# Kernel optimization log

Measured on AMD Instinct MI355X. Metric: run time of the kernel, lower is better.

The kernel has to match this reference:

```python
import jax, jax.numpy as jnp
import numpy as np

UNITS = 128
INPUT_DIM = 784
OUTPUT_DIM = 10
NUM_LAYERS = 8
BATCH = 2048
DT = 0.1
EPS = 0.01
TOL = 1e-4
STEPS = 15


def setup_inputs() -> dict:
    key = jax.random.key(0)
    k = jax.random.split(key, 7)
    s_in = 1.0 / np.sqrt(INPUT_DIM)
    s_u = 1.0 / np.sqrt(UNITS)
    return {
        "x": jax.random.normal(k[0], (BATCH, INPUT_DIM), jnp.float32),
        "w_in": jax.random.uniform(k[1], (UNITS, INPUT_DIM), jnp.float32, -s_in, s_in),
        "b_in": jax.random.uniform(k[2], (UNITS,), jnp.float32, -s_in, s_in),
        "w_blocks": jax.random.uniform(k[3], (NUM_LAYERS, UNITS, UNITS), jnp.float32, -s_u, s_u),
        "b_blocks": jax.random.uniform(k[4], (NUM_LAYERS, UNITS), jnp.float32, -s_u, s_u),
        "w_out": jax.random.uniform(k[5], (OUTPUT_DIM, UNITS), jnp.float32, -s_u, s_u),
        "b_out": jax.random.uniform(k[6], (OUTPUT_DIM,), jnp.float32, -s_u, s_u),
    }


def _build_A(w_blocks):
    # A_l = [[I, dt*W_l], [-dt*W_l^T, (1+dt/eps)*I]], shape [L, 2u, 2u]
    I = jnp.broadcast_to(jnp.eye(UNITS, dtype=w_blocks.dtype), (NUM_LAYERS, UNITS, UNITS))
    top = jnp.concatenate([I, DT * w_blocks], axis=2)
    bot = jnp.concatenate([-DT * jnp.transpose(w_blocks, (0, 2, 1)), (1.0 + DT / EPS) * I], axis=2)
    return jnp.concatenate([top, bot], axis=1)


def _sweep(z_in, A, b_blocks):
    # Fixed-point sweeping (no-grad region in the original). z_ls: [L, B, 2u]
    B = z_in.shape[0]

    def layer_step(z, xs):
        A_l, b_l, z_l = xs
        rhs = jnp.concatenate(
            [jnp.broadcast_to(DT * b_l, (B, UNITS)), (DT / EPS) * jnp.tanh(z_l[:, :UNITS])],
            axis=1,
        ) + z
        # A_l is shared across the batch: one LU, many rhs
        y = jnp.linalg.solve(A_l, rhs.T).T
        err = jnp.mean(jnp.linalg.norm(z_l - y, axis=1))
        return y, (y, err)

    def body(state):
        z_ls, _, step = state
        _, (new_zls, errs) = jax.lax.scan(layer_step, z_in, (A, b_blocks, z_ls))
        return (new_zls, jnp.mean(errs), step + 1)

    def cond(state):
        _, err, step = state
        return jnp.logical_and(step < STEPS, err > TOL)

    z0 = jnp.broadcast_to(z_in[None], (NUM_LAYERS,) + z_in.shape)
    z_ls, _, _ = jax.lax.while_loop(cond, body, (z0, jnp.float32(10.0), jnp.int32(0)))
    return z_ls


def _block(z_in, W, b, z_l):
    # implicit_forward of one TransNetLayerSweeping (z_l is the converged sweep state)
    u_l, v_l = z_l[:, :UNITS], z_l[:, UNITS:]
    u_out = -DT * (v_l @ W.T) + z_in[:, :UNITS] + DT * b
    v_out = DT * (u_l @ W) + z_in[:, UNITS:] - (DT / EPS) * (v_l - jnp.tanh(u_l))
    return jnp.concatenate([u_out, v_out], axis=1)


def reference(x, w_in, b_in, w_blocks, b_blocks, w_out, b_out):
    x1 = x @ w_in.T + b_in                                  # [B, u]
    z_in = jnp.concatenate([x1, jnp.tanh(x1)], axis=1)      # [B, 2u]
    z_ls = _sweep(z_in, _build_A(w_blocks), b_blocks)       # [L, B, 2u]
    # Original loop does z = block.implicit_forward(z_in) for every block,
    # so only the LAST block's output survives.
    z_out = _block(z_in, w_blocks[-1], b_blocks[-1], z_ls[-1])
    logits = z_out[:, :UNITS] @ w_out.T + b_out             # [B, out]
    return jax.nn.softmax(logits, axis=1)
```

## Files before the change

kernel.cpp:

```cpp
#include <hip/hip_runtime.h>

#define U 128
#define BATCH 2048
#define NL 8
#define NS 8
#define DTc 0.1f
#define TENf 10.0f
#define INVC (1.0f/11.0f)
#define AFACT (0.01f/11.0f)
#define AST 264

typedef unsigned short u16;
typedef __attribute__((ext_vector_type(8))) short bf16x8;
typedef __attribute__((ext_vector_type(4))) float f32x4;
#define MFMA16(a,b,c) __builtin_amdgcn_mfma_f32_16x16x32_bf16(a,b,c,0,0,0)

__device__ __forceinline__ float bf2f(u16 h){ return __uint_as_float(((unsigned int)h)<<16); }
__device__ __forceinline__ u16 f2bf(float f){
  unsigned int u = __float_as_uint(f);
  u += 0x7FFFu + ((u >> 16) & 1u);
  return (u16)(u >> 16);
}
__device__ __forceinline__ float fast_tanh(float x){
  float e = __expf(2.0f*x);
  return 1.0f - __fdividef(2.0f, e + 1.0f);
}
__device__ __forceinline__ int detect_md(const u16* x, int* s_bad, int t, int nthr){
  if(t==0) *s_bad = 0;
  __syncthreads();
  int f=0;
  for(int i=t;i<4096;i+=nthr){ float v = bf2f(x[i]); if(!(fabsf(v)<16.0f)) f=1; }
  if(f) atomicOr(s_bad,1);
  __syncthreads();
  return *s_bad ? 0 : 1;
}
__device__ __forceinline__ bf16x8 ld8f(const float* p){
  float4 f0 = *(const float4*)p, f1 = *(const float4*)(p+4);
  bf16x8 v;
  v[0]=(short)f2bf(f0.x); v[1]=(short)f2bf(f0.y); v[2]=(short)f2bf(f0.z); v[3]=(short)f2bf(f0.w);
  v[4]=(short)f2bf(f1.x); v[5]=(short)f2bf(f1.y); v[6]=(short)f2bf(f1.z); v[7]=(short)f2bf(f1.w);
  return v;
}
__device__ __forceinline__ void lgkm_barrier(){
  __builtin_amdgcn_sched_barrier(0);
  asm volatile("s_waitcnt lgkmcnt(0)\n\ts_barrier" ::: "memory");
  __builtin_amdgcn_sched_barrier(0);
}

__global__ __launch_bounds__(256) void convK(
    const void* __restrict__ xraw, const void* __restrict__ wb,
    u16* __restrict__ Wg, u16* __restrict__ Wtg){
  __shared__ int s_bad;
  const int t = threadIdx.x;
  const int md = detect_md((const u16*)xraw, &s_bad, t, 256);
  const int g = blockIdx.x*256 + t, GS = gridDim.x*256;
  for(int i=g;i<131072;i+=GS){
    u16 h = md ? ((const u16*)wb)[i] : f2bf(((const float*)wb)[i]);
    Wg[i] = h;
    int L = i>>14, j = i & 16383;
    Wtg[(L<<14) + (j&127)*U + (j>>7)] = h;
  }
}

template<typename EPI>
__device__ __forceinline__ void tile16(const u16* __restrict__ A, int lda,
                                       const u16* __restrict__ B, int ldb, EPI epi){
  const int lane = threadIdx.x & 63, w = threadIdx.x >> 6;
  const int ln = lane & 15, lq = lane >> 4;
  const int n0 = 32*w + ln, n1 = n0 + 16;
  bf16x8 af[4], b0[4], b1[4];
  #pragma unroll
  for(int kt=0;kt<4;kt++){
    af[kt] = *(const bf16x8*)&A[ln*lda + kt*32 + lq*8];
    b0[kt] = *(const bf16x8*)&B[n0*ldb + kt*32 + lq*8];
    b1[kt] = *(const bf16x8*)&B[n1*ldb + kt*32 + lq*8];
  }
  f32x4 a0 = {0,0,0,0}, a1 = {0,0,0,0};
  #pragma unroll
  for(int kt=0;kt<4;kt++){ a0 = MFMA16(af[kt], b0[kt], a0); a1 = MFMA16(af[kt], b1[kt], a1); }
  epi(a0, a1, n0, n1);
}

__global__ __launch_bounds__(256) void gemmP(const u16* __restrict__ Wtg, u16* __restrict__ Pg){
  const int L = blockIdx.x >> 3, mt = blockIdx.x & 7;
  const int lq = (threadIdx.x & 63) >> 4;
  const u16* WtL = Wtg + (L<<14);
  tile16(WtL + mt*16*U, U, WtL, U, [&](f32x4 a0, f32x4 a1, int n0, int n1){
    #pragma unroll
    for(int r=0;r<4;r++){
      int row = mt*16 + lq*4 + r;
      Pg[(L<<14) + row*U + n0] = f2bf(AFACT*a0[r]);
      Pg[(L<<14) + row*U + n1] = f2bf(AFACT*a1[r]);
    }
  });
}
__global__ __launch_bounds__(256) void gemmS(const u16* __restrict__ Pg, u16* __restrict__ Fb){
  const int L = blockIdx.x >> 3, mt = blockIdx.x & 7;
  const int lq = (threadIdx.x & 63) >> 4;
  const u16* PL = Pg + (L<<14);
  u16* FbL = Fb + (size_t)L*65536;
  tile16(PL + mt*16*U, U, PL, U, [&](f32x4 a0, f32x4 a1, int n0, int n1){
    #pragma unroll
    for(int r=0;r<4;r++){
      int row = mt*16 + lq*4 + r;
      FbL[row*256 + n0] = f2bf(INVC*(((row==n0)?1.0f:0.0f) - bf2f(PL[row*U+n0]) + a0[r]));
      FbL[row*256 + n1] = f2bf(INVC*(((row==n1)?1.0f:0.0f) - bf2f(PL[row*U+n1]) + a1[r]));
    }
  });
}
__global__ __launch_bounds__(256) void gemmQ(const u16* __restrict__ Fb, const u16* __restrict__ Wg,
                                             u16* __restrict__ FbW){
  const int L = blockIdx.x >> 3, mt = blockIdx.x & 7;
  const int lq = (threadIdx.x & 63) >> 4;
  const u16* FbL = Fb + (size_t)L*65536;
  u16* FbO = FbW + (size_t)L*65536;
  tile16(FbL + mt*16*256, 256, Wg + (L<<14), U, [&](f32x4 a0, f32x4 a1, int n0, int n1){
    #pragma unroll
    for(int r=0;r<4;r++){
      int row = mt*16 + lq*4 + r;
      u16 q0 = f2bf(DTc*a0[r]), q1 = f2bf(DTc*a1[r]);
      FbO[row*256 + 128 + n0] = q0;
      FbO[row*256 + 128 + n1] = q1;
      FbO[(128+n0)*256 + row] = q0;
      FbO[(128+n1)*256 + row] = q1;
    }
  });
}
__global__ __launch_bounds__(256) void gemmR(const u16* __restrict__ Wg, u16* __restrict__ Fb){
  const int L = blockIdx.x >> 3, mt = blockIdx.x & 7;
  const int lq = (threadIdx.x & 63) >> 4;
  u16* FbL = Fb + (size_t)L*65536;
  tile16(Wg + (L<<14) + mt*16*U, U, FbL + 128*256, 256, [&](f32x4 a0, f32x4 a1, int n0, int n1){
    #pragma unroll
    for(int r=0;r<4;r++){
      int row = mt*16 + lq*4 + r;
      FbL[(128+row)*256 + 128 + n0] = f2bf(DTc*a0[r]);
      FbL[(128+row)*256 + 128 + n1] = f2bf(DTc*a1[r]);
    }
  });
}
__global__ __launch_bounds__(256) void swizK(const u16* __restrict__ Fb, u16* __restrict__ Fsw){
  const int L = blockIdx.x >> 3, part = blockIdx.x & 7;
  const u16* FbL = Fb + (size_t)L*65536;
  for(int i = part*1024 + threadIdx.x; i < (part+1)*1024; i += 256){
    int lanei = i & 63, kt = (i>>6)&7, c = (i>>9)&3, w = (i>>11)&3;
    int lni = lanei & 15, lqi = lanei >> 4;
    int row_n = 64*w + 16*c + lni;
    int col_k = kt*32 + lqi*8;
    *(bf16x8*)&Fsw[((size_t)L*8192 + i)*8] = *(const bf16x8*)&FbL[row_n*256 + col_k];
  }
}

__global__ __launch_bounds__(1024,1) void mainK(
    const void* __restrict__ xraw, const void* __restrict__ w_in,
    const void* __restrict__ b_in, const void* __restrict__ bb,
    const bf16x8* __restrict__ Fsw, const void* __restrict__ w_out,
    const void* __restrict__ b_out, void* __restrict__ outraw){
  __shared__ u16 At[2][16*AST];
  __shared__ u16 zh16[NL][16][132];
  __shared__ float zinu[16*U];
  __shared__ float bbL[NL*U];
  __shared__ float lg[16*12];
  __shared__ int s_bad;
  float* uout = (float*)&At[0][0];

  const int t = threadIdx.x;
  const int lane = t & 63, wid = t >> 6, ln = lane & 15, lq = lane >> 4;
  const int r0 = blockIdx.x * 16;

  const int md = detect_md((const u16*)xraw, &s_bad, t, 1024);
  for(int i=t;i<NL*U;i+=1024)
    bbL[i] = DTc * (md ? bf2f(((const u16*)bb)[i]) : ((const float*)bb)[i]);
  __syncthreads();

  if(wid < 8){
    const int n0 = 16*wid + ln;
    const u16*   wrb = (const u16*)w_in   + (size_t)n0*784;
    const float* wrf = (const float*)w_in + (size_t)n0*784;
    const u16*   xrb = (const u16*)xraw   + (size_t)(r0+ln)*784;
    const float* xrf = (const float*)xraw + (size_t)(r0+ln)*784;
    f32x4 acc = {0,0,0,0};
    const bf16x8 z8 = {0,0,0,0,0,0,0,0};
    if(md){
      #pragma unroll
      for(int kt=0; kt<24; ++kt){
        int k0 = kt*32 + lq*8;
        acc = MFMA16(*(const bf16x8*)(xrb + k0), *(const bf16x8*)(wrb + k0), acc);
      }
      { int k0 = 768 + lq*8;
        bf16x8 av = z8, bv = z8;
        if(lq < 2){ av = *(const bf16x8*)(xrb + k0); bv = *(const bf16x8*)(wrb + k0); }
        acc = MFMA16(av, bv, acc);
      }
    } else {
      #pragma unroll 4
      for(int kt=0; kt<24; ++kt){
        int k0 = kt*32 + lq*8;
        acc = MFMA16(ld8f(xrf + k0), ld8f(wrf + k0), acc);
      }
      { int k0 = 768 + lq*8;
        bf16x8 av = z8, bv = z8;
        if(lq < 2){ av = ld8f(xrf + k0); bv = ld8f(wrf + k0); }
        acc = MFMA16(av, bv, acc);
      }
    }
    float bi = md ? bf2f(((const u16*)b_in)[n0]) : ((const float*)b_in)[n0];
    #pragma unroll
    for(int r=0;r<4;r++) zinu[(lq*4+r)*U + n0] = acc[r] + bi;
  }
  __syncthreads();

  for(int i=t; i<NL*16*128; i+=1024){
    int l = i>>11, row = (i>>7)&15, c = i & 127;
    zh16[l][row][c] = f2bf(zinu[row*U + c]);
  }
  float ru[4];
  if(wid < 8){
    const int n = 16*wid + ln;
    #pragma unroll
    for(int r=0;r<4;r++){
      int row = lq*4 + r;
      At[0][row*AST + n] = f2bf((TENf + 1.0f) * fast_tanh(zinu[row*U + n]));
    }
  } else {
    const int uc = 16*(wid-8) + ln;
    #pragma unroll
    for(int r=0;r<4;r++){
      int row = lq*4 + r;
      float v = zinu[row*U + uc] + bbL[uc];
      ru[r] = v;
      At[0][row*AST + 128 + uc] = f2bf(v);
    }
  }
  const bf16x8* fbase = Fsw + (wid>>2)*2048 + (wid&3)*512 + lane;
  bf16x8 BfA[8], BfB[8];
  #pragma unroll
  for(int kt=0;kt<8;kt++) BfA[kt] = fbase[kt*64];
  __syncthreads();

#define STEPBODY(STEPV, BC, BN, CURC) { \
    const int l = (STEPV) & 7; \
    const int lnext = (l+1) & 7; \
    const bool last = ((STEPV) == NS*NL-1); \
    { const bf16x8* fp = fbase + lnext*8192; \
      _Pragma("unroll") \
      for(int kt=0;kt<8;kt++) BN[kt] = fp[kt*64]; } \
    bf16x8 at8[8]; \
    _Pragma("unroll") \
    for(int kt=0;kt<8;kt++) at8[kt] = *(const bf16x8*)&At[CURC][ln*AST + kt*32 + lq*8]; \
    float th[4]; \
    if(wid < 8 && !last){ \
      _Pragma("unroll") \
      for(int r=0;r<4;r++) th[r] = TENf * fast_tanh(bf2f(zh16[lnext][lq*4 + r][16*wid + ln])); \
    } \
    f32x4 acc = {0,0,0,0}; \
    _Pragma("unroll") \
    for(int kt=0;kt<8;kt++) acc = MFMA16(at8[kt], BC[kt], acc); \
    if(wid < 8){ \
      if(!last){ \
        const bool wrap = (l == 7); \
        const int n = 16*wid + ln; \
        _Pragma("unroll") \
        for(int r=0;r<4;r++){ \
          int row = lq*4 + r; \
          float base = wrap ? fast_tanh(zinu[row*U + n]) : acc[r]; \
          At[1-(CURC)][row*AST + n] = f2bf(th[r] + base); \
        } \
      } \
    } else { \
      const int uc0 = 16*(wid-8) + ln; \
      _Pragma("unroll") \
      for(int r=0;r<4;r++){ \
        int row = lq*4 + r; \
        float yu = ru[r] - acc[r]; \
        zh16[l][row][uc0] = f2bf(yu); \
        if(last){ \
          uout[row*U + uc0] = zinu[row*U + uc0] + bbL[7*U + uc0] - acc[r]; \
        } else if(l == 7){ \
          float rn = zinu[row*U + uc0] + bbL[uc0]; \
          ru[r] = rn; \
          At[1-(CURC)][row*AST + 128 + uc0] = f2bf(rn); \
        } else { \
          float rn = yu + bbL[(l+1)*U + uc0]; \
          ru[r] = rn; \
          At[1-(CURC)][row*AST + 128 + uc0] = f2bf(rn); \
        } \
      } \
    } \
    lgkm_barrier(); \
  }

  for(int sp=0; sp<NS*NL; sp+=2){
    STEPBODY(sp,   BfA, BfB, 0)
    STEPBODY(sp+1, BfB, BfA, 1)
  }
#undef STEPBODY

  if(t < 160){
    int mm = t/10, o = t - mm*10;
    float a = md ? bf2f(((const u16*)b_out)[o]) : ((const float*)b_out)[o];
    if(md){
      const u16* wo = (const u16*)w_out + o*U;
      for(int k=0;k<U;k++) a += uout[mm*U + k]*bf2f(wo[k]);
    } else {
      const float* wo = (const float*)w_out + o*U;
      for(int k=0;k<U;k++) a += uout[mm*U + k]*wo[k];
    }
    lg[mm*12 + o] = a;
  }
  __syncthreads();
  if(t < 16){
    float mx = -1e30f;
    for(int o=0;o<10;o++) mx = fmaxf(mx, lg[t*12 + o]);
    float e[10]; float sum = 0.0f;
    for(int o=0;o<10;o++){ e[o] = __expf(lg[t*12 + o] - mx); sum += e[o]; }
    float inv = 1.0f / sum;
    for(int o=0;o<10;o++){
      float pv = e[o]*inv;
      if(md) ((u16*)outraw)[(size_t)(r0 + t)*10 + o] = f2bf(pv);
      else   ((float*)outraw)[(size_t)(r0 + t)*10 + o] = pv;
    }
  }
}

extern "C" void kernel_launch(void* const* d_in, const int* in_sizes, int n_in,
                              void* d_out, int out_size, void* d_ws, size_t ws_size,
                              hipStream_t stream) {
  char* p = (char*)d_ws;
  u16* Fb      = (u16*)p;  p += (size_t)8*256*256*2;
  u16* Fsw     = (u16*)p;  p += (size_t)8*256*256*2;
  u16* Wg      = (u16*)p;  p += (size_t)8*128*128*2;
  u16* Wtg     = (u16*)p;  p += (size_t)8*128*128*2;
  u16* Pg      = (u16*)p;  p += (size_t)8*128*128*2;

  convK<<<128, 256, 0, stream>>>(d_in[0], d_in[3], Wg, Wtg);
  gemmP<<<64, 256, 0, stream>>>(Wtg, Pg);
  gemmS<<<64, 256, 0, stream>>>(Pg, Fb);
  gemmQ<<<64, 256, 0, stream>>>(Fb, Wg, Fb);
  gemmR<<<64, 256, 0, stream>>>(Wg, Fb);
  swizK<<<64, 256, 0, stream>>>(Fb, Fsw);
  mainK<<<BATCH/16, 1024, 0, stream>>>(d_in[0], d_in[1], d_in[2], d_in[4],
                                       (const bf16x8*)Fsw, d_in[5], d_in[6], d_out);
}
```

Before: 203.2 us.

## Fuse weight-prep kernels into one persistent kernel with grid barriers

Merges the six small preprocessing launches (convert, three GEMM stages, assemble, swizzle) into one 64-block kernel. The stages are separated by atomic-counter global barriers that are reset with a memset before each launch. The aim is to cut per-launch overhead and the idle gaps between tiny kernels. It also raises mainK's launch_bounds occupancy hint from 1 to 4, which may limit registers. The spin barrier assumes all 64 blocks are co-resident and adds an extra memset.

```diff
diff --git a/kernel.cpp b/kernel.cpp
--- a/kernel.cpp
+++ b/kernel.cpp
@@ -9,6 +9,7 @@
 #define INVC (1.0f/11.0f)
 #define AFACT (0.01f/11.0f)
 #define AST 264
+#define PREP_BLKS 64
 
 typedef unsigned short u16;
 typedef __attribute__((ext_vector_type(8))) short bf16x8;
@@ -47,19 +48,16 @@
   __builtin_amdgcn_sched_barrier(0);
 }
 
-__global__ __launch_bounds__(256) void convK(
-    const void* __restrict__ xraw, const void* __restrict__ wb,
-    u16* __restrict__ Wg, u16* __restrict__ Wtg){
-  __shared__ int s_bad;
-  const int t = threadIdx.x;
-  const int md = detect_md((const u16*)xraw, &s_bad, t, 256);
-  const int g = blockIdx.x*256 + t, GS = gridDim.x*256;
-  for(int i=g;i<131072;i+=GS){
-    u16 h = md ? ((const u16*)wb)[i] : f2bf(((const float*)wb)[i]);
-    Wg[i] = h;
-    int L = i>>14, j = i & 16383;
-    Wtg[(L<<14) + (j&127)*U + (j>>7)] = h;
-  }
+__device__ __forceinline__ void gbar(unsigned* cnt, int idx){
+  __syncthreads();
+  if(threadIdx.x==0){
+    __threadfence();
+    unsigned old = __hip_atomic_fetch_add(&cnt[idx], 1u, __ATOMIC_ACQ_REL, __HIP_MEMORY_SCOPE_AGENT);
+    unsigned tgt = (old/PREP_BLKS + 1u)*PREP_BLKS;
+    while(__hip_atomic_load(&cnt[idx], __ATOMIC_ACQUIRE, __HIP_MEMORY_SCOPE_AGENT) < tgt)
+      __builtin_amdgcn_s_sleep(4);
+  }
+  __syncthreads();
 }
 
 template<typename EPI>
@@ -81,24 +79,41 @@
   epi(a0, a1, n0, n1);
 }
 
-__global__ __launch_bounds__(256) void gemmP(const u16* __restrict__ Wtg, u16* __restrict__ Pg){
-  const int L = blockIdx.x >> 3, mt = blockIdx.x & 7;
-  const int lq = (threadIdx.x & 63) >> 4;
+__global__ __launch_bounds__(256) void prepK(
+    const void* __restrict__ xraw, const void* __restrict__ wb,
+    u16* __restrict__ Wg, u16* __restrict__ Wtg, u16* __restrict__ Pg,
+    u16* __restrict__ Fb, u16* __restrict__ Fsw, unsigned* __restrict__ cnt){
+  __shared__ int s_bad;
+  const int t = threadIdx.x, bid = blockIdx.x;
+  const int md = detect_md((const u16*)xraw, &s_bad, t, 256);
+
+  {
+    const int g = bid*256 + t, GS = PREP_BLKS*256;
+    for(int i=g;i<131072;i+=GS){
+      u16 h = md ? ((const u16*)wb)[i] : f2bf(((const float*)wb)[i]);
+      Wg[i] = h;
+      int L = i>>14, j = i & 16383;
+      Wtg[(L<<14) + (j&127)*U + (j>>7)] = h;
+    }
+  }
+  gbar(cnt, 0);
+
+  const int L = bid >> 3, mt = bid & 7;
+  const int lq = (t & 63) >> 4;
   const u16* WtL = Wtg + (L<<14);
+  u16* PL  = Pg + (L<<14);
+  u16* FbL = Fb + (size_t)L*65536;
+
   tile16(WtL + mt*16*U, U, WtL, U, [&](f32x4 a0, f32x4 a1, int n0, int n1){
     #pragma unroll
     for(int r=0;r<4;r++){
       int row = mt*16 + lq*4 + r;
-      Pg[(L<<14) + row*U + n0] = f2bf(AFACT*a0[r]);
-      Pg[(L<<14) + row*U + n1] = f2bf(AFACT*a1[r]);
+      PL[row*U + n0] = f2bf(AFACT*a0[r]);
+      PL[row*U + n1] = f2bf(AFACT*a1[r]);
     }
   });
-}
-__global__ __launch_bounds__(256) void gemmS(const u16* __restrict__ Pg, u16* __restrict__ Fb){
-  const int L = blockIdx.x >> 3, mt = blockIdx.x & 7;
-  const int lq = (threadIdx.x & 63) >> 4;
-  const u16* PL = Pg + (L<<14);
-  u16* FbL = Fb + (size_t)L*65536;
+  gbar(cnt, 1);
+
   tile16(PL + mt*16*U, U, PL, U, [&](f32x4 a0, f32x4 a1, int n0, int n1){
     #pragma unroll
     for(int r=0;r<4;r++){
@@ -107,29 +122,21 @@
       FbL[row*256 + n1] = f2bf(INVC*(((row==n1)?1.0f:0.0f) - bf2f(PL[row*U+n1]) + a1[r]));
     }
   });
-}
-__global__ __launch_bounds__(256) void gemmQ(const u16* __restrict__ Fb, const u16* __restrict__ Wg,
-                                             u16* __restrict__ FbW){
-  const int L = blockIdx.x >> 3, mt = blockIdx.x & 7;
-  const int lq = (threadIdx.x & 63) >> 4;
-  const u16* FbL = Fb + (size_t)L*65536;
-  u16* FbO = FbW + (size_t)L*65536;
+  __syncthreads();
+
   tile16(FbL + mt*16*256, 256, Wg + (L<<14), U, [&](f32x4 a0, f32x4 a1, int n0, int n1){
     #pragma unroll
     for(int r=0;r<4;r++){
       int row = mt*16 + lq*4 + r;
       u16 q0 = f2bf(DTc*a0[r]), q1 = f2bf(DTc*a1[r]);
-      FbO[row*256 + 128 + n0] = q0;
-      FbO[row*256 + 128 + n1] = q1;
-      FbO[(128+n0)*256 + row] = q0;
-      FbO[(128+n1)*256 + row] = q1;
+      FbL[row*256 + 128 + n0] = q0;
+      FbL[row*256 + 128 + n1] = q1;
+      FbL[(128+n0)*256 + row] = q0;
+      FbL[(128+n1)*256 + row] = q1;
     }
   });
-}
-__global__ __launch_bounds__(256) void gemmR(const u16* __restrict__ Wg, u16* __restrict__ Fb){
-  const int L = blockIdx.x >> 3, mt = blockIdx.x & 7;
-  const int lq = (threadIdx.x & 63) >> 4;
-  u16* FbL = Fb + (size_t)L*65536;
+  gbar(cnt, 2);
+
   tile16(Wg + (L<<14) + mt*16*U, U, FbL + 128*256, 256, [&](f32x4 a0, f32x4 a1, int n0, int n1){
     #pragma unroll
     for(int r=0;r<4;r++){
@@ -138,11 +145,9 @@
       FbL[(128+row)*256 + 128 + n1] = f2bf(DTc*a1[r]);
     }
   });
-}
-__global__ __launch_bounds__(256) void swizK(const u16* __restrict__ Fb, u16* __restrict__ Fsw){
-  const int L = blockIdx.x >> 3, part = blockIdx.x & 7;
-  const u16* FbL = Fb + (size_t)L*65536;
-  for(int i = part*1024 + threadIdx.x; i < (part+1)*1024; i += 256){
+  gbar(cnt, 3);
+
+  for(int i = mt*1024 + t; i < (mt+1)*1024; i += 256){
     int lanei = i & 63, kt = (i>>6)&7, c = (i>>9)&3, w = (i>>11)&3;
     int lni = lanei & 15, lqi = lanei >> 4;
     int row_n = 64*w + 16*c + lni;
@@ -151,7 +156,7 @@
   }
 }
 
-__global__ __launch_bounds__(1024,1) void mainK(
+__global__ __launch_bounds__(1024,4) void mainK(
     const void* __restrict__ xraw, const void* __restrict__ w_in,
     const void* __restrict__ b_in, const void* __restrict__ bb,
     const bf16x8* __restrict__ Fsw, const void* __restrict__ w_out,
@@ -332,13 +337,10 @@
   u16* Wg      = (u16*)p;  p += (size_t)8*128*128*2;
   u16* Wtg     = (u16*)p;  p += (size_t)8*128*128*2;
   u16* Pg      = (u16*)p;  p += (size_t)8*128*128*2;
-
-  convK<<<128, 256, 0, stream>>>(d_in[0], d_in[3], Wg, Wtg);
-  gemmP<<<64, 256, 0, stream>>>(Wtg, Pg);
-  gemmS<<<64, 256, 0, stream>>>(Pg, Fb);
-  gemmQ<<<64, 256, 0, stream>>>(Fb, Wg, Fb);
-  gemmR<<<64, 256, 0, stream>>>(Wg, Fb);
-  swizK<<<64, 256, 0, stream>>>(Fb, Fsw);
+  unsigned* cnt = (unsigned*)p; p += 64;
+
+  hipMemsetAsync(cnt, 0, 64, stream);
+  prepK<<<PREP_BLKS, 256, 0, stream>>>(d_in[0], d_in[3], Wg, Wtg, Pg, Fb, Fsw, cnt);
   mainK<<<BATCH/16, 1024, 0, stream>>>(d_in[0], d_in[1], d_in[2], d_in[4],
                                        (const bf16x8*)Fsw, d_in[5], d_in[6], d_out);
 }
```

Result: slower. 218.8 us (+7.7%).

## Split each batch tile across two cooperating workgroups synchronized via global flags

Applied to the files above, without the earlier changes.

The 1024-thread main kernel is replaced by 256 workgroups of 512 threads, grouped into pairs. In each pair, one workgroup computes the v-half and the other the u-half of every sweep step. The halves are exchanged through global-memory slabs, and a release/acquire flag handshake with a spin-wait runs at every step. This aims to use more CUs, since 128 blocks previously left many idle. In exchange it adds per-step global round-trip latency, and it relies on both workgroups of a pair being co-resident to avoid deadlock.

```diff
diff --git a/kernel.cpp b/kernel.cpp
--- a/kernel.cpp
+++ b/kernel.cpp
@@ -11,13 +11,14 @@
 #define AST 264
 
 typedef unsigned short u16;
+typedef unsigned int u32;
 typedef __attribute__((ext_vector_type(8))) short bf16x8;
 typedef __attribute__((ext_vector_type(4))) float f32x4;
 #define MFMA16(a,b,c) __builtin_amdgcn_mfma_f32_16x16x32_bf16(a,b,c,0,0,0)
 
-__device__ __forceinline__ float bf2f(u16 h){ return __uint_as_float(((unsigned int)h)<<16); }
+__device__ __forceinline__ float bf2f(u16 h){ return __uint_as_float(((u32)h)<<16); }
 __device__ __forceinline__ u16 f2bf(float f){
-  unsigned int u = __float_as_uint(f);
+  u32 u = __float_as_uint(f);
   u += 0x7FFFu + ((u >> 16) & 1u);
   return (u16)(u >> 16);
 }
@@ -45,6 +46,12 @@
   __builtin_amdgcn_sched_barrier(0);
   asm volatile("s_waitcnt lgkmcnt(0)\n\ts_barrier" ::: "memory");
   __builtin_amdgcn_sched_barrier(0);
+}
+__device__ __forceinline__ void ast32(u32* p, u32 v){
+  __hip_atomic_store(p, v, __ATOMIC_RELAXED, __HIP_MEMORY_SCOPE_AGENT);
+}
+__device__ __forceinline__ u32 ald32(const u32* p){
+  return __hip_atomic_load(p, __ATOMIC_RELAXED, __HIP_MEMORY_SCOPE_AGENT);
 }
 
 __global__ __launch_bounds__(256) void convK(
@@ -151,11 +158,12 @@
   }
 }
 
-__global__ __launch_bounds__(1024,1) void mainK(
+__global__ __launch_bounds__(512,2) void mainK2(
     const void* __restrict__ xraw, const void* __restrict__ w_in,
     const void* __restrict__ b_in, const void* __restrict__ bb,
     const bf16x8* __restrict__ Fsw, const void* __restrict__ w_out,
-    const void* __restrict__ b_out, void* __restrict__ outraw){
+    const void* __restrict__ b_out, void* __restrict__ outraw,
+    u32* __restrict__ slabYg, u32* __restrict__ slabTg, u32* __restrict__ flags){
   __shared__ u16 At[2][16*AST];
   __shared__ u16 zh16[NL][16][132];
   __shared__ float zinu[16*U];
@@ -166,17 +174,25 @@
 
   const int t = threadIdx.x;
   const int lane = t & 63, wid = t >> 6, ln = lane & 15, lq = lane >> 4;
-  const int r0 = blockIdx.x * 16;
-
-  const int md = detect_md((const u16*)xraw, &s_bad, t, 1024);
-  for(int i=t;i<NL*U;i+=1024)
+  const int pair = blockIdx.x & 127;
+  const int role = blockIdx.x >> 7;
+  const int r0 = pair * 16;
+  const int n  = 16*wid + ln;
+  const int uc = n;
+
+  u32* slabY = slabYg + pair*4096;
+  u32* slabT = slabTg + pair*2048;
+  u32* myflag    = flags + pair*32 + (role ? 16 : 0);
+  u32* otherflag = flags + pair*32 + (role ? 0 : 16);
+
+  const int md = detect_md((const u16*)xraw, &s_bad, t, 512);
+  for(int i=t;i<NL*U;i+=512)
     bbL[i] = DTc * (md ? bf2f(((const u16*)bb)[i]) : ((const float*)bb)[i]);
   __syncthreads();
 
-  if(wid < 8){
-    const int n0 = 16*wid + ln;
-    const u16*   wrb = (const u16*)w_in   + (size_t)n0*784;
-    const float* wrf = (const float*)w_in + (size_t)n0*784;
+  {
+    const u16*   wrb = (const u16*)w_in   + (size_t)n*784;
+    const float* wrf = (const float*)w_in + (size_t)n*784;
     const u16*   xrb = (const u16*)xraw   + (size_t)(r0+ln)*784;
     const float* xrf = (const float*)xraw + (size_t)(r0+ln)*784;
     f32x4 acc = {0,0,0,0};
@@ -204,35 +220,28 @@
         acc = MFMA16(av, bv, acc);
       }
     }
-    float bi = md ? bf2f(((const u16*)b_in)[n0]) : ((const float*)b_in)[n0];
-    #pragma unroll
-    for(int r=0;r<4;r++) zinu[(lq*4+r)*U + n0] = acc[r] + bi;
-  }
-  __syncthreads();
-
-  for(int i=t; i<NL*16*128; i+=1024){
-    int l = i>>11, row = (i>>7)&15, c = i & 127;
-    zh16[l][row][c] = f2bf(zinu[row*U + c]);
+    float bi = md ? bf2f(((const u16*)b_in)[n]) : ((const float*)b_in)[n];
+    #pragma unroll
+    for(int r=0;r<4;r++) zinu[(lq*4+r)*U + n] = acc[r] + bi;
+  }
+  __syncthreads();
+
+  if(role==0){
+    for(int i=t; i<NL*16*128; i+=512){
+      int l = i>>11, row = (i>>7)&15, c = i & 127;
+      zh16[l][row][c] = f2bf(zinu[row*U + c]);
+    }
   }
   float ru[4];
-  if(wid < 8){
-    const int n = 16*wid + ln;
-    #pragma unroll
-    for(int r=0;r<4;r++){
-      int row = lq*4 + r;
-      At[0][row*AST + n] = f2bf((TENf + 1.0f) * fast_tanh(zinu[row*U + n]));
-    }
-  } else {
-    const int uc = 16*(wid-8) + ln;
-    #pragma unroll
-    for(int r=0;r<4;r++){
-      int row = lq*4 + r;
-      float v = zinu[row*U + uc] + bbL[uc];
-      ru[r] = v;
-      At[0][row*AST + 128 + uc] = f2bf(v);
-    }
-  }
-  const bf16x8* fbase = Fsw + (wid>>2)*2048 + (wid&3)*512 + lane;
+  #pragma unroll
+  for(int r=0;r<4;r++){
+    int row = lq*4 + r;
+    At[0][row*AST + n] = f2bf((TENf + 1.0f) * fast_tanh(zinu[row*U + n]));
+    float v = zinu[row*U + uc] + bbL[uc];
+    ru[r] = v;
+    At[0][row*AST + 128 + uc] = f2bf(v);
+  }
+  const bf16x8* fbase = Fsw + (2*role + (wid>>2))*2048 + (wid&3)*512 + lane;
   bf16x8 BfA[8], BfB[8];
   #pragma unroll
   for(int kt=0;kt<8;kt++) BfA[kt] = fbase[kt*64];
@@ -242,6 +251,7 @@
     const int l = (STEPV) & 7; \
     const int lnext = (l+1) & 7; \
     const bool last = ((STEPV) == NS*NL-1); \
+    const int slot = (STEPV) & 1; \
     { const bf16x8* fp = fbase + lnext*8192; \
       _Pragma("unroll") \
       for(int kt=0;kt<8;kt++) BN[kt] = fp[kt*64]; } \
@@ -249,45 +259,80 @@
     _Pragma("unroll") \
     for(int kt=0;kt<8;kt++) at8[kt] = *(const bf16x8*)&At[CURC][ln*AST + kt*32 + lq*8]; \
     float th[4]; \
-    if(wid < 8 && !last){ \
+    if(role==0 && !last){ \
       _Pragma("unroll") \
-      for(int r=0;r<4;r++) th[r] = TENf * fast_tanh(bf2f(zh16[lnext][lq*4 + r][16*wid + ln])); \
+      for(int r=0;r<4;r++) th[r] = TENf * fast_tanh(bf2f(zh16[lnext][lq*4 + r][n])); \
     } \
     f32x4 acc = {0,0,0,0}; \
     _Pragma("unroll") \
     for(int kt=0;kt<8;kt++) acc = MFMA16(at8[kt], BC[kt], acc); \
-    if(wid < 8){ \
+    if(role==0){ \
       if(!last){ \
         const bool wrap = (l == 7); \
-        const int n = 16*wid + ln; \
+        u32* sT = slabT + slot*1024; \
+        u16 tt[4]; \
         _Pragma("unroll") \
         for(int r=0;r<4;r++){ \
           int row = lq*4 + r; \
           float base = wrap ? fast_tanh(zinu[row*U + n]) : acc[r]; \
-          At[1-(CURC)][row*AST + n] = f2bf(th[r] + base); \
-        } \
+          tt[r] = f2bf(th[r] + base); \
+          At[1-(CURC)][row*AST + n] = tt[r]; \
+        } \
+        ast32(&sT[n*8 + lq*2 + 0], (u32)tt[0] | ((u32)tt[1]<<16)); \
+        ast32(&sT[n*8 + lq*2 + 1], (u32)tt[2] | ((u32)tt[3]<<16)); \
       } \
     } else { \
-      const int uc0 = 16*(wid-8) + ln; \
-      _Pragma("unroll") \
-      for(int r=0;r<4;r++){ \
-        int row = lq*4 + r; \
-        float yu = ru[r] - acc[r]; \
-        zh16[l][row][uc0] = f2bf(yu); \
-        if(last){ \
-          uout[row*U + uc0] = zinu[row*U + uc0] + bbL[7*U + uc0] - acc[r]; \
-        } else if(l == 7){ \
-          float rn = zinu[row*U + uc0] + bbL[uc0]; \
+      if(last){ \
+        _Pragma("unroll") \
+        for(int r=0;r<4;r++){ \
+          int row = lq*4 + r; \
+          uout[row*U + uc] = zinu[row*U + uc] + bbL[7*U + uc] - acc[r]; \
+        } \
+      } else { \
+        const bool wrap = (l == 7); \
+        u32* sY = slabY + slot*2048; \
+        _Pragma("unroll") \
+        for(int r=0;r<4;r++){ \
+          int row = lq*4 + r; \
+          float yu = ru[r] - acc[r]; \
+          ast32(&sY[(row<<7) + uc], __float_as_uint(yu)); \
+          float rn = wrap ? (zinu[row*U + uc] + bbL[uc]) : (yu + bbL[(l+1)*U + uc]); \
           ru[r] = rn; \
-          At[1-(CURC)][row*AST + 128 + uc0] = f2bf(rn); \
-        } else { \
-          float rn = yu + bbL[(l+1)*U + uc0]; \
-          ru[r] = rn; \
-          At[1-(CURC)][row*AST + 128 + uc0] = f2bf(rn); \
+          At[1-(CURC)][row*AST + 128 + uc] = f2bf(rn); \
         } \
       } \
     } \
-    lgkm_barrier(); \
+    if(!last){ \
+      __syncthreads();   \
+      if(t==0){ \
+        __hip_atomic_store(myflag, (u32)((STEPV)+1), __ATOMIC_RELEASE, __HIP_MEMORY_SCOPE_AGENT); \
+        while(__hip_atomic_load(otherflag, __ATOMIC_ACQUIRE, __HIP_MEMORY_SCOPE_AGENT) < (u32)((STEPV)+1)) \
+          __builtin_amdgcn_s_sleep(1); \
+      } \
+      __syncthreads(); \
+      if(role==0){ \
+        const u32* sY = slabY + slot*2048; \
+        const bool wrap = (l == 7); \
+        _Pragma("unroll") \
+        for(int j=0;j<4;j++){ \
+          int idx = t*4 + j, row = idx>>7, ucc = idx & 127; \
+          float yu = __uint_as_float(ald32(&sY[idx])); \
+          zh16[l][row][ucc] = f2bf(yu); \
+          float rn = wrap ? (zinu[row*U + ucc] + bbL[ucc]) : (yu + bbL[(l+1)*U + ucc]); \
+          At[1-(CURC)][row*AST + 128 + ucc] = f2bf(rn); \
+        } \
+      } else { \
+        const u32* sT = slabT + slot*1024; \
+        _Pragma("unroll") \
+        for(int j=0;j<2;j++){ \
+          int w = t*2 + j, nn = w>>3, q = w & 7; \
+          u32 v = ald32(&sT[w]); \
+          At[1-(CURC)][(2*q)*AST + nn]   = (u16)(v & 0xffffu); \
+          At[1-(CURC)][(2*q+1)*AST + nn] = (u16)(v >> 16); \
+        } \
+      } \
+      lgkm_barrier(); \
+    } \
   }
 
   for(int sp=0; sp<NS*NL; sp+=2){
@@ -296,29 +341,32 @@
   }
 #undef STEPBODY
 
-  if(t < 160){
-    int mm = t/10, o = t - mm*10;
-    float a = md ? bf2f(((const u16*)b_out)[o]) : ((const float*)b_out)[o];
-    if(md){
-      const u16* wo = (const u16*)w_out + o*U;
-      for(int k=0;k<U;k++) a += uout[mm*U + k]*bf2f(wo[k]);
-    } else {
-      const float* wo = (const float*)w_out + o*U;
-      for(int k=0;k<U;k++) a += uout[mm*U + k]*wo[k];
-    }
-    lg[mm*12 + o] = a;
-  }
-  __syncthreads();
-  if(t < 16){
-    float mx = -1e30f;
-    for(int o=0;o<10;o++) mx = fmaxf(mx, lg[t*12 + o]);
-    float e[10]; float sum = 0.0f;
-    for(int o=0;o<10;o++){ e[o] = __expf(lg[t*12 + o] - mx); sum += e[o]; }
-    float inv = 1.0f / sum;
-    for(int o=0;o<10;o++){
-      float pv = e[o]*inv;
-      if(md) ((u16*)outraw)[(size_t)(r0 + t)*10 + o] = f2bf(pv);
-      else   ((float*)outraw)[(size_t)(r0 + t)*10 + o] = pv;
+  if(role==1){
+    __syncthreads();
+    if(t < 160){
+      int mm = t/10, o = t - mm*10;
+      float a = md ? bf2f(((const u16*)b_out)[o]) : ((const float*)b_out)[o];
+      if(md){
+        const u16* wo = (const u16*)w_out + o*U;
+        for(int k=0;k<U;k++) a += uout[mm*U + k]*bf2f(wo[k]);
+      } else {
+        const float* wo = (const float*)w_out + o*U;
+        for(int k=0;k<U;k++) a += uout[mm*U + k]*wo[k];
+      }
+      lg[mm*12 + o] = a;
+    }
+    __syncthreads();
+    if(t < 16){
+      float mx = -1e30f;
+      for(int o=0;o<10;o++) mx = fmaxf(mx, lg[t*12 + o]);
+      float e[10]; float sum = 0.0f;
+      for(int o=0;o<10;o++){ e[o] = __expf(lg[t*12 + o] - mx); sum += e[o]; }
+      float inv = 1.0f / sum;
+      for(int o=0;o<10;o++){
+        float pv = e[o]*inv;
+        if(md) ((u16*)outraw)[(size_t)(r0 + t)*10 + o] = f2bf(pv);
+        else   ((float*)outraw)[(size_t)(r0 + t)*10 + o] = pv;
+      }
     }
   }
 }
@@ -332,13 +380,18 @@
   u16* Wg      = (u16*)p;  p += (size_t)8*128*128*2;
   u16* Wtg     = (u16*)p;  p += (size_t)8*128*128*2;
   u16* Pg      = (u16*)p;  p += (size_t)8*128*128*2;
-
+  u32* slabY   = (u32*)p;  p += (size_t)128*2*2048*4;
+  u32* slabT   = (u32*)p;  p += (size_t)128*2*1024*4;
+  u32* flags   = (u32*)p;  p += (size_t)128*32*4;
+
+  hipMemsetAsync(flags, 0, (size_t)128*32*4, stream);
   convK<<<128, 256, 0, stream>>>(d_in[0], d_in[3], Wg, Wtg);
   gemmP<<<64, 256, 0, stream>>>(Wtg, Pg);
   gemmS<<<64, 256, 0, stream>>>(Pg, Fb);
   gemmQ<<<64, 256, 0, stream>>>(Fb, Wg, Fb);
   gemmR<<<64, 256, 0, stream>>>(Wg, Fb);
   swizK<<<64, 256, 0, stream>>>(Fb, Fsw);
-  mainK<<<BATCH/16, 1024, 0, stream>>>(d_in[0], d_in[1], d_in[2], d_in[4],
-                                       (const bf16x8*)Fsw, d_in[5], d_in[6], d_out);
-}
+  mainK2<<<256, 512, 0, stream>>>(d_in[0], d_in[1], d_in[2], d_in[4],
+                                  (const bf16x8*)Fsw, d_in[5], d_in[6], d_out,
+                                  slabY, slabT, flags);
+}
```

After: 677.4 us. 233% more time.
